# Performance work log

Hardware: AMD Instinct MI355X
Metric: run time of the kernel (lower is better)

The kernel has to match this reference:

```python
import jax, jax.numpy as jnp
import numpy as np
from jax.scipy.special import logsumexp

LOG2PI = float(np.log(2.0 * np.pi))
N_GRID = 25  # dim == 2 -> N = 25
NEG = -1e9


def _cond_logprob(cand, hist_loc, hist_t, t, beta, sigma):
    # cand [B,M,d], hist_loc [B,H,d], hist_t [B,H], t [B]
    d = cand.shape[-1]
    logw = -beta * (t[:, None] - hist_t)                       # [B,H]
    logw = logw - logsumexp(logw, axis=1, keepdims=True)
    diff = cand[:, :, None, :] - hist_loc[:, None, :, :]       # [B,M,H,d]
    sq = jnp.sum(diff * diff, axis=-1)                         # [B,M,H]
    logN = -0.5 * sq / (sigma * sigma) - d * jnp.log(sigma) - 0.5 * d * LOG2PI
    return logsumexp(logw[:, None, :] + logN, axis=-1)         # [B,M]


def _gmm_call(times, locs, beta, sigma):
    # causal GMM loglik: event k explained by mixture over events j<k
    B, L, d = locs.shape
    dt = times[:, :, None] - times[:, None, :]                 # [B,L,L]
    mask = jnp.tril(jnp.ones((L, L), dtype=bool), -1)          # j < k
    raw = jnp.where(mask, -beta * dt, NEG)
    logw = raw - logsumexp(raw, axis=-1, keepdims=True)
    diff = locs[:, :, None, :] - locs[:, None, :, :]           # [B,L,L,d]
    sq = jnp.sum(diff * diff, axis=-1)
    logN = -0.5 * sq / (sigma * sigma) - d * jnp.log(sigma) - 0.5 * d * LOG2PI
    logp = logsumexp(jnp.where(mask, logw + logN, NEG), axis=-1)  # [B,L]
    logp0 = -0.5 * jnp.sum(locs[:, 0] ** 2, axis=-1) - 0.5 * d * LOG2PI
    return logp0 + jnp.sum(logp[:, 1:], axis=-1)               # [B]


def setup_inputs() -> dict:
    key = jax.random.key(0)
    ks = jax.random.split(key, 6)
    B, H, PLTS, D = 64, 384, 16, 2
    input_time = jnp.sort(jax.random.uniform(ks[0], (B, H), dtype=jnp.float32), axis=1)
    curr_time = 1.0 + jnp.sort(jax.random.uniform(ks[1], (B, PLTS), dtype=jnp.float32), axis=1)
    history_data = jax.random.normal(ks[2], (B, H, D), dtype=jnp.float32)
    expected_data = jax.random.normal(ks[3], (B, PLTS, D), dtype=jnp.float32)
    aux_state_in = jax.random.normal(ks[4], (B, H, 1), dtype=jnp.float32)
    aux_state_out = jax.random.normal(ks[5], (B, PLTS, 1), dtype=jnp.float32)
    beta = jnp.ones((1,), dtype=jnp.float32)
    log_sigma = jnp.zeros((1,), dtype=jnp.float32)
    return {"curr_time": curr_time, "input_time": input_time,
            "history_data": history_data, "expected_data": expected_data,
            "aux_state_in": aux_state_in, "aux_state_out": aux_state_out,
            "beta": beta, "log_sigma": log_sigma}


def reference(curr_time, input_time, history_data, expected_data,
              aux_state_in, aux_state_out, beta, log_sigma):
    sigma = jnp.exp(log_sigma)
    B, plts, d = expected_data.shape
    hist = history_data
    times = input_time
    preds = []
    for i in range(plts):
        expected_loc = expected_data[:, i, :]                  # [B,d]
        nd = jnp.concatenate([hist, expected_loc[:, None, :]], axis=1)  # [B,H+1,d]
        # faithful to source: bounds from event rows 0 and 1 (scalar min/max)
        minx, maxx = jnp.min(nd[:, 0]), jnp.max(nd[:, 0])
        miny, maxy = jnp.min(nd[:, 1]), jnp.max(nd[:, 1])
        xlim = jnp.linspace(minx, maxx, N_GRID)
        ylim = jnp.linspace(miny, maxy, N_GRID)
        X1, X2 = jnp.meshgrid(xlim, ylim)
        arr = jnp.stack([X1.reshape(-1), X2.reshape(-1)], axis=1)  # [N*N,2]
        cand = jnp.broadcast_to(arr[None], (B, N_GRID * N_GRID, 2))
        ll = _cond_logprob(cand, hist, times, curr_time[:, i], beta, sigma)  # [B,N*N]
        arg = jnp.argmin(ll, axis=-1)                          # [B]
        predicted = jnp.take_along_axis(cand, arg[:, None, None], axis=1)[:, 0, :]  # [B,2]
        preds.append(predicted)
        hist = jnp.concatenate([hist, predicted[:, None, :]], axis=1)
        times = jnp.concatenate([times, curr_time[:, i:i + 1]], axis=1)
    spatial_loglik = _gmm_call(times, hist, beta, sigma)       # [B]
    predicted_out = jnp.stack(preds, axis=0)                   # [plts,B,2]
    return spatial_loglik, predicted_out
```

## Files before the change

### kernel.cpp

```cpp
#include <hip/hip_runtime.h>
#include <hip/hip_bf16.h>
#include <math.h>

#define BB    64
#define HH    384
#define PLTS  16
#define LMAX  (HH + PLTS)
#define NG    25
#define NC    (NG * NG)
#define BLOCK 1024
#define NWAVES (BLOCK / 64)
#define FSTR  388
#define NCHUNK 8
#define KC    48
#define GEMM_UNITS (125 * NCHUNK)

#if defined(__has_builtin) && __has_builtin(__builtin_amdgcn_exp2f)
static __device__ __forceinline__ float fast_exp2(float x) { return __builtin_amdgcn_exp2f(x); }
#else
static __device__ __forceinline__ float fast_exp2(float x) { return exp2f(x); }
#endif
#if defined(__has_builtin) && __has_builtin(__builtin_amdgcn_logf)
static __device__ __forceinline__ float fast_log2(float x) { return __builtin_amdgcn_logf(x); }
#else
static __device__ __forceinline__ float fast_log2(float x) { return log2f(x); }
#endif

#if defined(__has_builtin)
#if __has_builtin(__builtin_amdgcn_update_dpp) && __has_builtin(__builtin_amdgcn_readlane)
#define HAS_DPP 1
#endif
#endif

static __device__ __forceinline__ float wave_min_all(float v) {
#ifdef HAS_DPP
    float r = v;
    #define DPP_STEP(ctrl) { int ri = __float_as_int(r); \
        int si = __builtin_amdgcn_update_dpp(ri, ri, (ctrl), 0xf, 0xf, false); \
        r = fminf(r, __int_as_float(si)); }
    DPP_STEP(0x111) DPP_STEP(0x112) DPP_STEP(0x114) DPP_STEP(0x118)
    DPP_STEP(0x142) DPP_STEP(0x143)
    #undef DPP_STEP
    return __int_as_float(__builtin_amdgcn_readlane(__float_as_int(r), 63));
#else
    for (int o = 1; o < 64; o <<= 1) v = fminf(v, __shfl_xor(v, o, 64));
    return v;
#endif
}

static __device__ __forceinline__ int lane_bcast_int(int x, int src_lane) {
#ifdef HAS_DPP
    return __builtin_amdgcn_readlane(x, src_lane);
#else
    return __shfl(x, src_lane, 64);
#endif
}

__global__ __launch_bounds__(BLOCK)
void spatio_kernel(const float* __restrict__ ct,
                   const float* __restrict__ it,
                   const float* __restrict__ hd,
                   const float* __restrict__ beta_p,
                   const float* __restrict__ lsig_p,
                   float* __restrict__ out)
{
    __shared__ __align__(16) float FxT[NG][FSTR];
    __shared__ __align__(16) float FyT[NG][FSTR];
    __shared__ __align__(16) float u_s [LMAX];
    __shared__ __align__(16) float px_s[LMAX];
    __shared__ __align__(16) float py_s[LMAX];
    __shared__ float  w2s[LMAX];
    __shared__ float2 hxy[LMAX];
    __shared__ __align__(16) float P[NC * NCHUNK];
    __shared__ float  Pg[BLOCK];
    __shared__ float  rowt[16];
    __shared__ float  pre[LMAX];
    __shared__ float  wsum[NWAVES];
    __shared__ float  rv[NWAVES];
    __shared__ float  sb[4];

    const int b    = blockIdx.x;
    const int tid  = threadIdx.x;
    const int lane = tid & 63;
    const int wave = tid >> 6;

    const float LOG2E  = 1.4426950408889634f;
    const float LN2    = 0.69314718055994531f;
    const float LOG2PI = 1.8378770664093453f;
    const float INF    = __builtin_inff();

    const float beta  = beta_p[0];
    const float lsig  = lsig_p[0];
    const float sigma = fast_exp2(lsig * LOG2E);
    const float cc    = -0.5f / (sigma * sigma);
    const float c2    = cc * LOG2E;
    const float bl    = beta * LOG2E;
    const float Sc    = -2.0f * lsig - LOG2PI;

    for (int j = tid; j < HH; j += BLOCK) {
        float t = it[b * HH + j];
        float x = hd[(b * HH + j) * 2 + 0];
        float y = hd[(b * HH + j) * 2 + 1];
        float w = bl * t;
        w2s[j]  = w;
        hxy[j]  = make_float2(x, y);
        u_s[j]  = fmaf(c2, x * x + y * y, w);
        px_s[j] = -2.0f * c2 * x;
        py_s[j] = -2.0f * c2 * y;
    }

    float wn_r[16];
    if (wave == 0) {
        const float4* ct4 = (const float4*)(ct + b * PLTS);
        float4 c0 = ct4[0], c1 = ct4[1], c2v = ct4[2], c3 = ct4[3];
        wn_r[0]=bl*c0.x;  wn_r[1]=bl*c0.y;  wn_r[2]=bl*c0.z;  wn_r[3]=bl*c0.w;
        wn_r[4]=bl*c1.x;  wn_r[5]=bl*c1.y;  wn_r[6]=bl*c1.z;  wn_r[7]=bl*c1.w;
        wn_r[8]=bl*c2v.x; wn_r[9]=bl*c2v.y; wn_r[10]=bl*c2v.z;wn_r[11]=bl*c2v.w;
        wn_r[12]=bl*c3.x; wn_r[13]=bl*c3.y; wn_r[14]=bl*c3.z; wn_r[15]=bl*c3.w;
    } else {
        #pragma unroll
        for (int k = 0; k < 16; ++k) wn_r[k] = 0.0f;
    }

    if (tid < 64) {
        const float* p = hd + tid * (HH * 2);
        float p0x = p[0], p0y = p[1], p1x = p[2], p1y = p[3];
        float xmn = fminf(p0x, p0y), xmx = fmaxf(p0x, p0y);
        float ymn = fminf(p1x, p1y), ymx = fmaxf(p1x, p1y);
        for (int o = 32; o > 0; o >>= 1) {
            xmn = fminf(xmn, __shfl_down(xmn, o, 64));
            xmx = fmaxf(xmx, __shfl_down(xmx, o, 64));
            ymn = fminf(ymn, __shfl_down(ymn, o, 64));
            ymx = fmaxf(ymx, __shfl_down(ymx, o, 64));
        }
        if (tid == 0) { sb[0] = xmn; sb[1] = xmx; sb[2] = ymn; sb[3] = ymx; }
    }
    __syncthreads();

    const float minx = sb[0], maxx = sb[1], miny = sb[2], maxy = sb[3];
    const float stepx = (maxx - minx) * (1.0f / 24.0f);
    const float stepy = (maxy - miny) * (1.0f / 24.0f);

    for (int idx = tid; idx < NG * HH; idx += BLOCK) {
        int row = idx / HH;
        int j   = idx - row * HH;
        float2 h = hxy[j];
        float cxr = fmaf((float)row, stepx, minx);
        float cyr = fmaf((float)row, stepy, miny);
        float dx = cxr - h.x;
        float dy = cyr - h.y;
        FxT[row][j] = fast_exp2(fmaf(c2 * dx, dx, w2s[j]));
        FyT[row][j] = fast_exp2(c2 * dy * dy);
    }
    __syncthreads();

    if (tid < GEMM_UNITS) {
        int chunk = tid / 125;
        int r     = tid - chunk * 125;
        int ky    = r / 5;
        int kxg   = r - ky * 5;
        const int g0 = chunk * (KC / 4);
        const float4* fy4 = (const float4*)&FyT[ky][0];
        const float4* fx0 = (const float4*)&FxT[5 * kxg + 0][0];
        const float4* fx1 = (const float4*)&FxT[5 * kxg + 1][0];
        const float4* fx2 = (const float4*)&FxT[5 * kxg + 2][0];
        const float4* fx3 = (const float4*)&FxT[5 * kxg + 3][0];
        const float4* fx4 = (const float4*)&FxT[5 * kxg + 4][0];
        float4 A0 = {0,0,0,0}, A1 = {0,0,0,0}, A2 = {0,0,0,0}, A3 = {0,0,0,0}, A4 = {0,0,0,0};
        #pragma unroll
        for (int g = g0; g < g0 + KC / 4; ++g) {
            float4 bv = fy4[g];
            float4 x0 = fx0[g];
            A0.x = fmaf(x0.x, bv.x, A0.x); A0.y = fmaf(x0.y, bv.y, A0.y);
            A0.z = fmaf(x0.z, bv.z, A0.z); A0.w = fmaf(x0.w, bv.w, A0.w);
            float4 x1 = fx1[g];
            A1.x = fmaf(x1.x, bv.x, A1.x); A1.y = fmaf(x1.y, bv.y, A1.y);
            A1.z = fmaf(x1.z, bv.z, A1.z); A1.w = fmaf(x1.w, bv.w, A1.w);
            float4 x2 = fx2[g];
            A2.x = fmaf(x2.x, bv.x, A2.x); A2.y = fmaf(x2.y, bv.y, A2.y);
            A2.z = fmaf(x2.z, bv.z, A2.z); A2.w = fmaf(x2.w, bv.w, A2.w);
            float4 x3 = fx3[g];
            A3.x = fmaf(x3.x, bv.x, A3.x); A3.y = fmaf(x3.y, bv.y, A3.y);
            A3.z = fmaf(x3.z, bv.z, A3.z); A3.w = fmaf(x3.w, bv.w, A3.w);
            float4 x4 = fx4[g];
            A4.x = fmaf(x4.x, bv.x, A4.x); A4.y = fmaf(x4.y, bv.y, A4.y);
            A4.z = fmaf(x4.z, bv.z, A4.z); A4.w = fmaf(x4.w, bv.w, A4.w);
        }
        const int cb = 5 * kxg + 25 * ky;
        P[(cb + 0) * NCHUNK + chunk] = (A0.x + A0.y) + (A0.z + A0.w);
        P[(cb + 1) * NCHUNK + chunk] = (A1.x + A1.y) + (A1.z + A1.w);
        P[(cb + 2) * NCHUNK + chunk] = (A2.x + A2.y) + (A2.z + A2.w);
        P[(cb + 3) * NCHUNK + chunk] = (A3.x + A3.y) + (A3.z + A3.w);
        P[(cb + 4) * NCHUNK + chunk] = (A4.x + A4.y) + (A4.z + A4.w);
    }
    __syncthreads();

    if (wave == 0) {
        float Sv[10], cxk[10], cyk[10];
        const int cbase = lane * 10;
        #pragma unroll
        for (int k = 0; k < 10; ++k) {
            int c = cbase + k;
            if (c < NC) {
                const float4* p4 = (const float4*)&P[c * NCHUNK];
                float4 a = p4[0], d = p4[1];
                Sv[k] = ((a.x + a.y) + (a.z + a.w)) + ((d.x + d.y) + (d.z + d.w));
                int ky = (int)((c + 0.5f) * 0.04f);
                int kx = c - 25 * ky;
                cxk[k] = fmaf((float)kx, stepx, minx);
                cyk[k] = fmaf((float)ky, stepy, miny);
            } else {
                Sv[k] = INF; cxk[k] = 0.0f; cyk[k] = 0.0f;
            }
        }
        #pragma unroll
        for (int i = 0; i < PLTS; ++i) {
            float vl = Sv[0];
            #pragma unroll
            for (int k = 1; k < 10; ++k) vl = fminf(vl, Sv[k]);
            float vmin = wave_min_all(vl);
            unsigned long long m = __ballot(vl == vmin);
            int win = (int)__ffsll((unsigned long long)m) - 1;
            int kl = 9;
            #pragma unroll
            for (int k = 9; k >= 0; --k) if (Sv[k] == vmin) kl = k;
            int kwin = lane_bcast_int(kl, win);
            int idx  = win * 10 + kwin;
            int   ky = (int)((idx + 0.5f) * 0.04f);
            int   kx = idx - 25 * ky;
            float px = fmaf((float)kx, stepx, minx);
            float py = fmaf((float)ky, stepy, miny);
            float wn = wn_r[i];
            if (lane == 0) {
                const int L = HH + i;
                w2s[L]  = wn;
                hxy[L]  = make_float2(px, py);
                u_s[L]  = fmaf(c2, px * px + py * py, wn);
                px_s[L] = -2.0f * c2 * px;
                py_s[L] = -2.0f * c2 * py;
                out[BB + (i * BB + b) * 2 + 0] = px;
                out[BB + (i * BB + b) * 2 + 1] = py;
            }
            #pragma unroll
            for (int k = 0; k < 10; ++k) {
                float dx = px - cxk[k], dy = py - cyk[k];
                Sv[k] += fast_exp2(fmaf(c2, fmaf(dx, dx, dy * dy), wn));
            }
        }
    } else {
        const int t2 = tid - 64;
        int row = 0, c = 0;
        if (t2 < 100)      { row = t2 + 1; c = 0; }
        else if (t2 < 300) { int u = t2 - 100; row = 101 + (u >> 1); c = u & 1; }
        else if (t2 < 600) { int u = t2 - 300; int q = u / 3; row = 201 + q; c = u - 3 * q; }
        else if (t2 < 932) { int u = t2 - 600; row = 301 + (u >> 2); c = u & 3; }
        float part = 0.0f;
        if (row > 0) {
            int j0 = c * 100;
            int j1 = min(row, j0 + 100);
            float2 hi = hxy[row];
            float xi = hi.x, yi = hi.y;
            float Ai = c2 * fmaf(xi, xi, yi * yi);
            const float4* u4g  = (const float4*)u_s;
            const float4* px4g = (const float4*)px_s;
            const float4* py4g = (const float4*)py_s;
            float a0 = 0.f, a1 = 0.f, a2 = 0.f, a3 = 0.f;
            int j = j0;
            for (; j + 4 <= j1; j += 4) {
                int g = j >> 2;
                float4 U = u4g[g], PX = px4g[g], PY = py4g[g];
                a0 += fast_exp2(fmaf(PX.x, xi, fmaf(PY.x, yi, U.x + Ai)));
                a1 += fast_exp2(fmaf(PX.y, xi, fmaf(PY.y, yi, U.y + Ai)));
                a2 += fast_exp2(fmaf(PX.z, xi, fmaf(PY.z, yi, U.z + Ai)));
                a3 += fast_exp2(fmaf(PX.w, xi, fmaf(PY.w, yi, U.w + Ai)));
            }
            for (; j < j1; ++j)
                a0 += fast_exp2(fmaf(px_s[j], xi, fmaf(py_s[j], yi, u_s[j] + Ai)));
            part = (a0 + a1) + (a2 + a3);
        }
        Pg[tid] = part;
    }
    __syncthreads();

    {
        const int row = HH + wave;
        int j0 = lane * 7;
        int j1 = min(row, j0 + 7);
        float2 hi = hxy[row];
        float xi = hi.x, yi = hi.y;
        float Ai = c2 * fmaf(xi, xi, yi * yi);
        float part = 0.0f;
        for (int j = j0; j < j1; ++j)
            part += fast_exp2(fmaf(px_s[j], xi, fmaf(py_s[j], yi, u_s[j] + Ai)));
        for (int o = 32; o > 0; o >>= 1) part += __shfl_down(part, o, 64);
        if (lane == 0) rowt[wave] = part;
    }

    float x = (tid < LMAX) ? fast_exp2(w2s[tid]) : 0.0f;
    for (int o = 1; o < 64; o <<= 1) {
        float y = __shfl_up(x, o, 64);
        if (lane >= o) x += y;
    }
    if (lane == 63) wsum[wave] = x;
    __syncthreads();
    float off = 0.0f;
    for (int w = 0; w < wave; ++w) off += wsum[w];
    if (tid < LMAX) pre[tid] = x + off;
    __syncthreads();

    float acc = 0.0f;
    if (tid >= 1 && tid < LMAX) {
        const int row = tid;
        float tot;
        if (row <= 100)      { tot = Pg[64 + row - 1]; }
        else if (row <= 200) { int base = 64 + 100 + (row - 101) * 2;
                               tot = Pg[base] + Pg[base + 1]; }
        else if (row <= 300) { int base = 64 + 300 + (row - 201) * 3;
                               tot = Pg[base] + Pg[base + 1] + Pg[base + 2]; }
        else if (row <= 383) { int base = 64 + 600 + (row - 301) * 4;
                               tot = (Pg[base] + Pg[base + 1]) + (Pg[base + 2] + Pg[base + 3]); }
        else                 { tot = rowt[row - HH]; }
        acc = Sc + LN2 * (fast_log2(tot) - fast_log2(pre[row - 1]));
    }
    for (int o = 32; o > 0; o >>= 1) acc += __shfl_down(acc, o, 64);
    if (lane == 0) rv[wave] = acc;
    __syncthreads();
    if (tid == 0) {
        float tot = 0.0f;
        for (int w = 0; w < NWAVES; ++w) tot += rv[w];
        float2 h0 = hxy[0];
        tot += -0.5f * (h0.x * h0.x + h0.y * h0.y) - LOG2PI;
        out[b] = tot;
    }
}

extern "C" void kernel_launch(void* const* d_in, const int* in_sizes, int n_in,
                              void* d_out, int out_size, void* d_ws, size_t ws_size,
                              hipStream_t stream) {
    const float* ct   = (const float*)d_in[0];
    const float* it   = (const float*)d_in[1];
    const float* hd   = (const float*)d_in[2];
    const float* beta = (const float*)d_in[6];
    const float* lsig = (const float*)d_in[7];
    float* out = (float*)d_out;

    hipLaunchKernelGGL(spatio_kernel, dim3(BB), dim3(BLOCK), 0, stream,
                       ct, it, hd, beta, lsig, out);
}
```

Baseline: 81.62 us.

## Rebalance GMM row partition and move prefix-sum into idle wave during prediction loop

The static partition of historical GMM rows across worker threads is rebalanced into 120-wide chunks with a 96-wide last tier, so per-thread work is more even and fewer threads are used. The exclusive prefix sum of time weights is now computed by one otherwise idle wave during the serial prediction phase, because the prediction times are written into w2s up front from curr_time. This removes one block-wide barrier and the later scan. History loads are also vectorized as float2. The risk is that the new index mapping and the single-wave 7-per-lane scan must still cover exactly all 400 entries.

```diff
diff --git a/kernel.cpp b/kernel.cpp
--- a/kernel.cpp
+++ b/kernel.cpp
@@ -75,7 +75,6 @@
     __shared__ float  Pg[BLOCK];
     __shared__ float  rowt[16];
     __shared__ float  pre[LMAX];
-    __shared__ float  wsum[NWAVES];
     __shared__ float  rv[NWAVES];
     __shared__ float  sb[4];
 
@@ -97,17 +96,20 @@
     const float bl    = beta * LOG2E;
     const float Sc    = -2.0f * lsig - LOG2PI;
 
-    for (int j = tid; j < HH; j += BLOCK) {
-        float t = it[b * HH + j];
-        float x = hd[(b * HH + j) * 2 + 0];
-        float y = hd[(b * HH + j) * 2 + 1];
-        float w = bl * t;
-        w2s[j]  = w;
-        hxy[j]  = make_float2(x, y);
-        u_s[j]  = fmaf(c2, x * x + y * y, w);
-        px_s[j] = -2.0f * c2 * x;
-        py_s[j] = -2.0f * c2 * y;
-    }
+    {
+        const float2* hd2 = (const float2*)(hd + (size_t)b * HH * 2);
+        for (int j = tid; j < HH; j += BLOCK) {
+            float t  = it[b * HH + j];
+            float2 p = hd2[j];
+            float w  = bl * t;
+            w2s[j]  = w;
+            hxy[j]  = p;
+            u_s[j]  = fmaf(c2, p.x * p.x + p.y * p.y, w);
+            px_s[j] = -2.0f * c2 * p.x;
+            py_s[j] = -2.0f * c2 * p.y;
+        }
+    }
+    if (tid < PLTS) w2s[HH + tid] = bl * ct[b * PLTS + tid];
 
     float wn_r[16];
     if (wave == 0) {
@@ -233,7 +235,6 @@
             float wn = wn_r[i];
             if (lane == 0) {
                 const int L = HH + i;
-                w2s[L]  = wn;
                 hxy[L]  = make_float2(px, py);
                 u_s[L]  = fmaf(c2, px * px + py * py, wn);
                 px_s[L] = -2.0f * c2 * px;
@@ -249,36 +250,66 @@
         }
     } else {
         const int t2 = tid - 64;
-        int row = 0, c = 0;
-        if (t2 < 100)      { row = t2 + 1; c = 0; }
-        else if (t2 < 300) { int u = t2 - 100; row = 101 + (u >> 1); c = u & 1; }
-        else if (t2 < 600) { int u = t2 - 300; int q = u / 3; row = 201 + q; c = u - 3 * q; }
-        else if (t2 < 932) { int u = t2 - 600; row = 301 + (u >> 2); c = u & 3; }
-        float part = 0.0f;
-        if (row > 0) {
-            int j0 = c * 100;
-            int j1 = min(row, j0 + 100);
-            float2 hi = hxy[row];
-            float xi = hi.x, yi = hi.y;
-            float Ai = c2 * fmaf(xi, xi, yi * yi);
-            const float4* u4g  = (const float4*)u_s;
-            const float4* px4g = (const float4*)px_s;
-            const float4* py4g = (const float4*)py_s;
-            float a0 = 0.f, a1 = 0.f, a2 = 0.f, a3 = 0.f;
-            int j = j0;
-            for (; j + 4 <= j1; j += 4) {
-                int g = j >> 2;
-                float4 U = u4g[g], PX = px4g[g], PY = py4g[g];
-                a0 += fast_exp2(fmaf(PX.x, xi, fmaf(PY.x, yi, U.x + Ai)));
-                a1 += fast_exp2(fmaf(PX.y, xi, fmaf(PY.y, yi, U.y + Ai)));
-                a2 += fast_exp2(fmaf(PX.z, xi, fmaf(PY.z, yi, U.z + Ai)));
-                a3 += fast_exp2(fmaf(PX.w, xi, fmaf(PY.w, yi, U.w + Ai)));
-            }
-            for (; j < j1; ++j)
-                a0 += fast_exp2(fmaf(px_s[j], xi, fmaf(py_s[j], yi, u_s[j] + Ai)));
-            part = (a0 + a1) + (a2 + a3);
-        }
-        Pg[tid] = part;
+        if (t2 < 812) {
+            int row, c, csz;
+            if (t2 < 120)      { row = t2 + 1; c = 0; csz = 120; }
+            else if (t2 < 360) { int u = t2 - 120; row = 121 + (u >> 1); c = u & 1; csz = 120; }
+            else if (t2 < 720) { int u = t2 - 360; int q = u / 3; row = 241 + q; c = u - 3 * q; csz = 120; }
+            else               { int u = t2 - 720; row = 361 + (u >> 2); c = u & 3; csz = 96; }
+            int j0 = c * csz;
+            int j1 = min(row, j0 + csz);
+            float part = 0.0f;
+            {
+                float2 hi = hxy[row];
+                float xi = hi.x, yi = hi.y;
+                float Ai = c2 * fmaf(xi, xi, yi * yi);
+                const float4* u4g  = (const float4*)u_s;
+                const float4* px4g = (const float4*)px_s;
+                const float4* py4g = (const float4*)py_s;
+                float a0 = 0.f, a1 = 0.f, a2 = 0.f, a3 = 0.f;
+                int j = j0;
+                for (; j + 4 <= j1; j += 4) {
+                    int g = j >> 2;
+                    float4 U = u4g[g], PX = px4g[g], PY = py4g[g];
+                    a0 += fast_exp2(fmaf(PX.x, xi, fmaf(PY.x, yi, U.x + Ai)));
+                    a1 += fast_exp2(fmaf(PX.y, xi, fmaf(PY.y, yi, U.y + Ai)));
+                    a2 += fast_exp2(fmaf(PX.z, xi, fmaf(PY.z, yi, U.z + Ai)));
+                    a3 += fast_exp2(fmaf(PX.w, xi, fmaf(PY.w, yi, U.w + Ai)));
+                }
+                for (; j < j1; ++j)
+                    a0 += fast_exp2(fmaf(px_s[j], xi, fmaf(py_s[j], yi, u_s[j] + Ai)));
+                part = (a0 + a1) + (a2 + a3);
+            }
+            Pg[tid] = part;
+        } else if (t2 >= 896) {
+            const int i0 = lane * 7;
+            float e0=0,e1=0,e2=0,e3=0,e4=0,e5=0,e6=0;
+            float s = 0.0f;
+            if (i0 < LMAX) {
+                s = fast_exp2(w2s[i0]);                                e0 = s;
+                if (i0+1 < LMAX) { s += fast_exp2(w2s[i0+1]); }        e1 = s;
+                if (i0+2 < LMAX) { s += fast_exp2(w2s[i0+2]); }        e2 = s;
+                if (i0+3 < LMAX) { s += fast_exp2(w2s[i0+3]); }        e3 = s;
+                if (i0+4 < LMAX) { s += fast_exp2(w2s[i0+4]); }        e4 = s;
+                if (i0+5 < LMAX) { s += fast_exp2(w2s[i0+5]); }        e5 = s;
+                if (i0+6 < LMAX) { s += fast_exp2(w2s[i0+6]); }        e6 = s;
+            }
+            float inc = s;
+            for (int o = 1; o < 64; o <<= 1) {
+                float y = __shfl_up(inc, o, 64);
+                if (lane >= o) inc += y;
+            }
+            float off = inc - s;
+            if (i0 < LMAX) {
+                pre[i0] = e0 + off;
+                if (i0+1 < LMAX) pre[i0+1] = e1 + off;
+                if (i0+2 < LMAX) pre[i0+2] = e2 + off;
+                if (i0+3 < LMAX) pre[i0+3] = e3 + off;
+                if (i0+4 < LMAX) pre[i0+4] = e4 + off;
+                if (i0+5 < LMAX) pre[i0+5] = e5 + off;
+                if (i0+6 < LMAX) pre[i0+6] = e6 + off;
+            }
+        }
     }
     __syncthreads();
 
@@ -295,29 +326,18 @@
         for (int o = 32; o > 0; o >>= 1) part += __shfl_down(part, o, 64);
         if (lane == 0) rowt[wave] = part;
     }
-
-    float x = (tid < LMAX) ? fast_exp2(w2s[tid]) : 0.0f;
-    for (int o = 1; o < 64; o <<= 1) {
-        float y = __shfl_up(x, o, 64);
-        if (lane >= o) x += y;
-    }
-    if (lane == 63) wsum[wave] = x;
-    __syncthreads();
-    float off = 0.0f;
-    for (int w = 0; w < wave; ++w) off += wsum[w];
-    if (tid < LMAX) pre[tid] = x + off;
     __syncthreads();
 
     float acc = 0.0f;
     if (tid >= 1 && tid < LMAX) {
         const int row = tid;
         float tot;
-        if (row <= 100)      { tot = Pg[64 + row - 1]; }
-        else if (row <= 200) { int base = 64 + 100 + (row - 101) * 2;
+        if (row <= 120)      { tot = Pg[64 + row - 1]; }
+        else if (row <= 240) { int base = 64 + 120 + (row - 121) * 2;
                                tot = Pg[base] + Pg[base + 1]; }
-        else if (row <= 300) { int base = 64 + 300 + (row - 201) * 3;
+        else if (row <= 360) { int base = 64 + 360 + (row - 241) * 3;
                                tot = Pg[base] + Pg[base + 1] + Pg[base + 2]; }
-        else if (row <= 383) { int base = 64 + 600 + (row - 301) * 4;
+        else if (row <= 383) { int base = 64 + 720 + (row - 361) * 4;
                                tot = (Pg[base] + Pg[base + 1]) + (Pg[base + 2] + Pg[base + 3]); }
         else                 { tot = rowt[row - HH]; }
         acc = Sc + LN2 * (fast_log2(tot) - fast_log2(pre[row - 1]));
```

Result: no change. 81.91 us (+0.4%).
